# Performance work log

Hardware: AMD Instinct MI355X
Metric: run time of the kernel (lower is better)

## Reference

```python
import jax, jax.numpy as jnp
import numpy as np

B, S, D = 4, 2048, 1024
H = 16
HD = D // H  # 64


def setup_inputs() -> dict:
    key = jax.random.key(0)
    ks = jax.random.split(key, 6)
    scale = 1.0 / np.sqrt(D)
    return {
        "x": jax.random.normal(ks[0], (B, S, D), dtype=jnp.float32),
        "W_q": jax.random.normal(ks[1], (D, D), dtype=jnp.float32) * scale,
        "W_k": jax.random.normal(ks[2], (D, D), dtype=jnp.float32) * scale,
        "W_v": jax.random.normal(ks[3], (D, D), dtype=jnp.float32) * scale,
        "W_o": jax.random.normal(ks[4], (D, D), dtype=jnp.float32) * scale,
        "b_o": jax.random.normal(ks[5], (D,), dtype=jnp.float32) * 0.01,
    }


def reference(x, W_q, W_k, W_v, W_o, b_o):
    b, n, _ = x.shape
    # projections (Linear stores weight as [out,in]; here W_* are [in,out])
    q = (x @ W_q).reshape(b, n, H, HD).transpose(0, 2, 1, 3)  # [b,h,n,hd]
    k = (x @ W_k).reshape(b, n, H, HD).transpose(0, 2, 1, 3)
    v = (x @ W_v).reshape(b, n, H, HD).transpose(0, 2, 1, 3)
    scores = jnp.einsum("bhqd,bhkd->bhqk", q, k) / np.sqrt(HD).astype(np.float32)
    causal = jnp.tril(jnp.ones((n, n), dtype=bool))  # True = keep
    scores = jnp.where(causal, scores, -jnp.inf)
    weights = jax.nn.softmax(scores, axis=-1)
    ctx = jnp.einsum("bhqk,bhkd->bhqd", weights, v)
    ctx = ctx.transpose(0, 2, 1, 3).reshape(b, n, D)
    return ctx @ W_o + b_o
```

## Files before the change

### kernel.cpp

```cpp
#include <hip/hip_runtime.h>
#include <cstdint>

#define S_LEN 2048
#define D_MODEL 1024
#define NH 16
#define HDIM 64
#define BATCH 4

typedef __attribute__((ext_vector_type(8))) __bf16 bfrag;
typedef __attribute__((ext_vector_type(4))) float ffrag;

__device__ __forceinline__ unsigned short f2bf(float f) {
    union { float f; uint32_t u; } v; v.f = f;
    uint32_t u = v.u;
    u += 0x7fff + ((u >> 16) & 1);
    return (unsigned short)(u >> 16);
}

__device__ __forceinline__ bfrag ld_frag(const unsigned short* p) {
    union { uint4 u; bfrag b; } x;
    x.u = *(const uint4*)p;
    return x.b;
}

__device__ __forceinline__ float fast_exp2(float x) {
#if __has_builtin(__builtin_amdgcn_exp2f)
    return __builtin_amdgcn_exp2f(x);
#else
    return __expf(x * 0.6931471805599453f);
#endif
}

__device__ __forceinline__ uint32_t pack_bf16(float a, float b) {
    union { float f; uint32_t u; } x, y; x.f = a; y.f = b;
    return __builtin_amdgcn_perm(y.u + 0x8000u, x.u + 0x8000u, 0x07060302u);
}

__device__ __forceinline__ void g2l16(const unsigned short* g, unsigned short* l) {
    __builtin_amdgcn_global_load_lds(
        (const __attribute__((address_space(1))) void*)g,
        (__attribute__((address_space(3))) void*)l, 16, 0, 0);
}

__global__ __launch_bounds__(256) void prep_kernel(const float* __restrict__ x,
                                                   const float* __restrict__ w0,
                                                   const float* __restrict__ w1,
                                                   const float* __restrict__ w2,
                                                   const float* __restrict__ w3,
                                                   unsigned short* __restrict__ xb,
                                                   unsigned short* __restrict__ wt) {
    __shared__ float tile[32][33];
    int bid = blockIdx.x;
    int t = threadIdx.x;
    if (bid < 4096) {
        int i = bid * 256 + t;
        const float4* p = (const float4*)x + (size_t)i * 2;
        float4 a = p[0], b = p[1];
        union { unsigned short u[8]; uint4 v; } o;
        o.u[0]=f2bf(a.x); o.u[1]=f2bf(a.y); o.u[2]=f2bf(a.z); o.u[3]=f2bf(a.w);
        o.u[4]=f2bf(b.x); o.u[5]=f2bf(b.y); o.u[6]=f2bf(b.z); o.u[7]=f2bf(b.w);
        ((uint4*)xb)[i] = o.v;
    } else {
        int r = bid - 4096;
        int mat = r >> 10;
        int rem = r & 1023;
        const float* w = (mat == 0) ? w0 : (mat == 1) ? w1 : (mat == 2) ? w2 : w3;
        int n0 = (rem & 31) * 32, k0 = (rem >> 5) * 32;
        int tx = t & 31, ty = t >> 5;
        for (int i = 0; i < 32; i += 8)
            tile[ty + i][tx] = w[(size_t)(k0 + ty + i) * D_MODEL + n0 + tx];
        __syncthreads();
        unsigned short* o = wt + (size_t)mat * D_MODEL * D_MODEL;
        for (int i = 0; i < 32; i += 8)
            o[(size_t)(n0 + ty + i) * D_MODEL + (k0 + tx)] = f2bf(tile[tx][ty + i]);
    }
}

#define MFMA_BF16 __builtin_amdgcn_mfma_f32_16x16x32_bf16

__device__ __forceinline__ int vb_idx(int row, int col) {
    return row * 64 + (col & 7) +
           ((((col >> 3) ^ ((row >> 2) & 3) ^ ((row >> 4) & 3)) & 7) << 3);
}

#define AS_SLOT 8192
#define NKT  (D_MODEL / 32)

template<int NF, int MODE>
__global__ __launch_bounds__(512, 4) void gemm_kernel(
    const unsigned short* __restrict__ A,
    const unsigned short* __restrict__ Bt,
    unsigned short* __restrict__ Qb,
    unsigned short* __restrict__ Kb,
    unsigned short* __restrict__ Vtb,
    float* __restrict__ Out,
    const float* __restrict__ bias) {
    constexpr int BN = NF * 32;
    constexpr int BS_SLOT = BN * 32;
    constexpr int NBCH = BN * 4;
    constexpr int NWB = NBCH / 64;
    __shared__ unsigned short Smem[3 * AS_SLOT + 3 * BS_SLOT];
    unsigned short* As = Smem;
    unsigned short* Bs = Smem + 3 * AS_SLOT;
    int t = threadIdx.x;

    int gx   = (int)gridDim.x;
    int nwg  = gx * (int)gridDim.y;
    int flat = (int)(blockIdx.y * gridDim.x + blockIdx.x);
    int cpx  = nwg >> 3;
    int wid  = (flat & 7) * cpx + (flat >> 3);
    int m0 = (wid / gx) * 256;
    int n0 = (wid % gx) * BN;

    int wave = t >> 6, lane = t & 63;
    int quad = lane >> 4, lrow = lane & 15;
    int wr = (wave & 3) * 64;
    int wc = (wave >> 2) * (NF * 16);

    ffrag acc[4][NF];
    const ffrag fz = {0.f, 0.f, 0.f, 0.f};
#pragma unroll
    for (int i = 0; i < 4; i++)
#pragma unroll
        for (int j = 0; j < NF; j++) acc[i][j] = fz;

    int r0 = t >> 2,        g0 = (t & 3) ^ ((r0 >> 1) & 3);
    int c1 = 512 + t;
    int r1 = c1 >> 2,       g1 = (c1 & 3) ^ ((r1 >> 1) & 3);
    int cbi = t & (NBCH - 1);
    int rB = cbi >> 2,      gB = (cbi & 3) ^ ((rB >> 1) & 3);
    const unsigned short* pA0 = A  + (size_t)(m0 + r0) * D_MODEL + g0 * 8;
    const unsigned short* pA1 = A  + (size_t)(m0 + r1) * D_MODEL + g1 * 8;
    const unsigned short* pB0 = Bt + (size_t)(n0 + rB) * D_MODEL + gB * 8;
    unsigned short* lA0 = &As[(wave * 64) * 8];
    unsigned short* lA1 = &As[(512 + wave * 64) * 8];
    unsigned short* lB0 = &Bs[((wave & (NWB - 1)) * 64) * 8];

    g2l16(pA0, lA0);
    g2l16(pA1, lA1);
    g2l16(pB0, lB0);
    g2l16(pA0 + 32, lA0 + AS_SLOT);
    g2l16(pA1 + 32, lA1 + AS_SLOT);
    g2l16(pB0 + 32, lB0 + BS_SLOT);

    int aCur = 0, aNxt = AS_SLOT, aSpr = 2 * AS_SLOT;
    int bCur = 0, bNxt = BS_SLOT, bSpr = 2 * BS_SLOT;

    for (int kt = 0; kt < NKT - 1; ++kt) {
        asm volatile("s_waitcnt vmcnt(3)\n\ts_barrier" ::: "memory");
        __builtin_amdgcn_sched_barrier(0);
        if (kt + 2 < NKT) {
            int ko = (kt + 2) * 32;
            g2l16(pA0 + ko, lA0 + aSpr);
            g2l16(pA1 + ko, lA1 + aSpr);
            g2l16(pB0 + ko, lB0 + bSpr);
        }
        bfrag af[4], bf[NF];
#pragma unroll
        for (int ni = 0; ni < NF; ni++) {
            int row = wc + ni * 16 + lrow;
            bf[ni] = ld_frag(&Bs[bCur + row * 32 + ((quad ^ ((row >> 1) & 3)) * 8)]);
        }
#pragma unroll
        for (int mi = 0; mi < 4; mi++) {
            int row = wr + mi * 16 + lrow;
            af[mi] = ld_frag(&As[aCur + row * 32 + ((quad ^ ((row >> 1) & 3)) * 8)]);
        }
        __builtin_amdgcn_s_setprio(1);
#pragma unroll
        for (int mi = 0; mi < 4; mi++)
#pragma unroll
            for (int ni = 0; ni < NF; ni++)
                acc[mi][ni] = MFMA_BF16(af[mi], bf[ni], acc[mi][ni], 0, 0, 0);
        __builtin_amdgcn_s_setprio(0);
        int ta = aCur; aCur = aNxt; aNxt = aSpr; aSpr = ta;
        int tb = bCur; bCur = bNxt; bNxt = bSpr; bSpr = tb;
    }
    asm volatile("s_waitcnt vmcnt(0)\n\ts_barrier" ::: "memory");
    __builtin_amdgcn_sched_barrier(0);
    {
        bfrag af[4], bf[NF];
#pragma unroll
        for (int ni = 0; ni < NF; ni++) {
            int row = wc + ni * 16 + lrow;
            bf[ni] = ld_frag(&Bs[bCur + row * 32 + ((quad ^ ((row >> 1) & 3)) * 8)]);
        }
#pragma unroll
        for (int mi = 0; mi < 4; mi++) {
            int row = wr + mi * 16 + lrow;
            af[mi] = ld_frag(&As[aCur + row * 32 + ((quad ^ ((row >> 1) & 3)) * 8)]);
        }
#pragma unroll
        for (int mi = 0; mi < 4; mi++)
#pragma unroll
            for (int ni = 0; ni < NF; ni++)
                acc[mi][ni] = MFMA_BF16(af[mi], bf[ni], acc[mi][ni], 0, 0, 0);
    }

    if constexpr (MODE == 0) {
        int matid = n0 >> 10;
        if (matid == 2) {
            __syncthreads();
            unsigned short* Lw = &Smem[wave * (64 * 64)];
#pragma unroll
            for (int mi = 0; mi < 4; mi++)
#pragma unroll
                for (int ni = 0; ni < NF; ni++)
#pragma unroll
                    for (int r = 0; r < 4; r++)
                        Lw[vb_idx(mi * 16 + quad * 4 + r, ni * 16 + lrow)] =
                            f2bf(acc[mi][ni][r]);
            int h0 = ((n0 + wc) & 1023) >> 6;
            int bb = m0 >> 11;
            size_t bh = (size_t)bb * NH + h0;
            int sbase = (m0 + wr) & 2047;
            unsigned short* Vt = Vtb + bh * (size_t)HDIM * S_LEN;
#pragma unroll
            for (int p = 0; p < 4; p++) {
                int d  = (lane >> 2) + p * 16;
                int sc = (lane & 3) * 16;
                union { unsigned short u[16]; uint4 v[2]; } o;
#pragma unroll
                for (int i = 0; i < 16; i++) o.u[i] = Lw[vb_idx(sc + i, d)];
                unsigned short* dst = Vt + (size_t)d * S_LEN + sbase + sc;
                *(uint4*)(dst)     = o.v[0];
                *(uint4*)(dst + 8) = o.v[1];
            }
        } else {
#pragma unroll
            for (int mi = 0; mi < 4; mi++) {
                int row = m0 + wr + mi * 16 + quad * 4;
#pragma unroll
                for (int ni = 0; ni < NF; ni++) {
                    int col = n0 + wc + ni * 16 + lrow;
#pragma unroll
                    for (int r = 0; r < 4; r++) {
                        float v = acc[mi][ni][r];
                        int m = row + r;
                        int nn = col & 1023;
                        int h = nn >> 6, d = nn & 63;
                        int b = m >> 11, s = m & 2047;
                        size_t bh = (size_t)(b * NH + h);
                        if (matid == 0) Qb[(bh * S_LEN + s) * HDIM + d] = f2bf(v);
                        else            Kb[(bh * S_LEN + s) * HDIM + d] = f2bf(v);
                    }
                }
            }
        }
    } else {
#pragma unroll
        for (int mi = 0; mi < 4; mi++) {
            int row = m0 + wr + mi * 16 + quad * 4;
#pragma unroll
            for (int ni = 0; ni < NF; ni++) {
                int col = n0 + wc + ni * 16 + lrow;
#pragma unroll
                for (int r = 0; r < 4; r++) {
                    int m = row + r;
                    Out[(size_t)m * D_MODEL + col] = acc[mi][ni][r] + bias[col];
                }
            }
        }
    }
}

#define SCALE2 0.18033688f
#define CSHIFT 4.0f
#define KVBUF 4096

__global__ __launch_bounds__(256, 4) void attn_kernel(
    const unsigned short* __restrict__ Qb,
    const unsigned short* __restrict__ Kb,
    const unsigned short* __restrict__ Vtb,
    unsigned short* __restrict__ ctxb) {
    __shared__ unsigned short Ks[2 * KVBUF];
    __shared__ unsigned short Vs[2 * KVBUF];
    __shared__ unsigned short Ps[4 * 16 * 64];
    int flat = (int)(blockIdx.y * gridDim.x + blockIdx.x);
    int wid  = (flat & 7) * 128 + (flat >> 3);
    int bx = wid & 15;
    int bh = wid >> 4;
    int t = threadIdx.x;
    int wave = t >> 6, lane = t & 63;
    int quad = lane >> 4, lrow = lane & 15;
    int swz = lrow & 7;
    int ca = (quad ^ swz) * 8;
    int cb = ca ^ 32;

    union { uint4 u; bfrag b; } one_u;
    one_u.u.x = 0x3F803F80u; one_u.u.y = 0x3F803F80u;
    one_u.u.z = 0x3F803F80u; one_u.u.w = 0x3F803F80u;
    bfrag onef = one_u.b;

    const unsigned short* Qg = Qb + (size_t)bh * S_LEN * HDIM;
    const unsigned short* Kg = Kb + (size_t)bh * S_LEN * HDIM;
    const unsigned short* Vg = Vtb + (size_t)bh * HDIM * S_LEN;
    int b = bh >> 4, h = bh & 15;

    int c0 = t, c1 = 256 + t;
    int kr0 = c0 >> 3, kp0 = (c0 & 7) ^ (kr0 & 7);
    int kr1 = c1 >> 3, kp1 = (c1 & 7) ^ (kr1 & 7);
    const unsigned short* pK0 = Kg + (size_t)kr0 * HDIM + kp0 * 8;
    const unsigned short* pK1 = Kg + (size_t)kr1 * HDIM + kp1 * 8;
    const unsigned short* pV0 = Vg + (size_t)kr0 * S_LEN + kp0 * 8;
    const unsigned short* pV1 = Vg + (size_t)kr1 * S_LEN + kp1 * 8;
    unsigned short* lK0 = &Ks[(wave * 64) * 8];
    unsigned short* lK1 = &Ks[(256 + wave * 64) * 8];
    unsigned short* lV0 = &Vs[(wave * 64) * 8];
    unsigned short* lV1 = &Vs[(256 + wave * 64) * 8];
    unsigned short* Pw = &Ps[wave * 16 * 64];

    int x8 = (((lrow >> 1) & 3) << 1) | (((lrow >> 3) & 1) << 3);
    int ql = lane >> 3, cc = lane & 7;

    for (int ph = 0; ph < 2; ph++) {
        int qc = ph == 0 ? (31 - bx) : bx;
        int qw = qc * 64 + wave * 16;
        int nk = qc + 1;

        bfrag qf[2];
#pragma unroll
        for (int c = 0; c < 2; c++)
            qf[c] = ld_frag(Qg + (size_t)(qw + lrow) * HDIM + c * 32 + quad * 8);

        ffrag acc[4];
        ffrag acc_l;
        const ffrag fz = {0.f, 0.f, 0.f, 0.f};
#pragma unroll
        for (int d = 0; d < 4; d++) acc[d] = fz;
        acc_l = fz;

        __syncthreads();
        g2l16(pK0, lK0);
        g2l16(pK1, lK1);
        g2l16(pV0, lV0);
        g2l16(pV1, lV1);

        for (int kt = 0; kt < nk; kt++) {
            int kbase = kt * 64;
            int buf = (kt & 1) * KVBUF;
            __syncthreads();
            if (kt + 1 < nk) {
                int nb = ((kt + 1) & 1) * KVBUF;
                size_t krow_off = (size_t)(kbase + 64) * HDIM;
                g2l16(pK0 + krow_off, lK0 + nb);
                g2l16(pK1 + krow_off, lK1 + nb);
                g2l16(pV0 + kbase + 64, lV0 + nb);
                g2l16(pV1 + kbase + 64, lV1 + nb);
            }

            ffrag sf[4];
            __builtin_amdgcn_s_setprio(1);
#pragma unroll
            for (int ki = 0; ki < 4; ki++) {
                int krow = buf + (ki * 16 + lrow) * 64;
                bfrag ka = ld_frag(&Ks[krow + ca]);
                bfrag kb = ld_frag(&Ks[krow + cb]);
                ffrag s = fz;
                s = __builtin_amdgcn_mfma_f32_16x16x32_bf16(ka, qf[0], s, 0, 0, 0);
                s = __builtin_amdgcn_mfma_f32_16x16x32_bf16(kb, qf[1], s, 0, 0, 0);
                sf[ki] = s;
            }
            __builtin_amdgcn_s_setprio(0);

            int qg = qw + lrow;
            bool need_mask = (kt == nk - 1);
            float sv[16];
#pragma unroll
            for (int ki = 0; ki < 4; ki++)
#pragma unroll
                for (int r = 0; r < 4; r++) {
                    float v = sf[ki][r];
                    if (need_mask) {
                        int key = kbase + ki * 16 + quad * 4 + r;
                        v = (key <= qg) ? v : -3.0e38f;
                    }
                    sv[ki * 4 + r] = fast_exp2(__builtin_fmaf(v, SCALE2, -CSHIFT));
                }
            int prow = lrow * 64;
#pragma unroll
            for (int ki = 0; ki < 4; ki++) {
                uint2 w2;
                w2.x = pack_bf16(sv[ki * 4 + 0], sv[ki * 4 + 1]);
                w2.y = pack_bf16(sv[ki * 4 + 2], sv[ki * 4 + 3]);
                int pc = ((ki * 2 + (quad >> 1)) ^ swz) * 8 + (quad & 1) * 4;
                *(uint2*)&Pw[prow + pc] = w2;
            }

            bfrag pf0 = ld_frag(&Pw[prow + ca]);
            bfrag pf1 = ld_frag(&Pw[prow + cb]);
            acc_l = __builtin_amdgcn_mfma_f32_16x16x32_bf16(onef, pf0, acc_l, 0, 0, 0);
            acc_l = __builtin_amdgcn_mfma_f32_16x16x32_bf16(onef, pf1, acc_l, 0, 0, 0);
            __builtin_amdgcn_s_setprio(1);
#pragma unroll
            for (int di = 0; di < 4; di++) {
                int vrow = buf + (di * 16 + lrow) * 64;
                bfrag va = ld_frag(&Vs[vrow + ca]);
                bfrag vb = ld_frag(&Vs[vrow + cb]);
                acc[di] = __builtin_amdgcn_mfma_f32_16x16x32_bf16(va, pf0, acc[di], 0, 0, 0);
                acc[di] = __builtin_amdgcn_mfma_f32_16x16x32_bf16(vb, pf1, acc[di], 0, 0, 0);
            }
            __builtin_amdgcn_s_setprio(0);
        }

        float rl = __builtin_amdgcn_rcpf(acc_l[0]);
#pragma unroll
        for (int di = 0; di < 4; di++) {
            uint2 w2;
            w2.x = pack_bf16(acc[di][0] * rl, acc[di][1] * rl);
            w2.y = pack_bf16(acc[di][2] * rl, acc[di][3] * rl);
            int slot = (4 * di + quad) ^ x8;
            *(uint2*)&Pw[lrow * 64 + slot * 4] = w2;
        }
#pragma unroll
        for (int p = 0; p < 2; p++) {
            int r = p * 8 + ql;
            int rx = ((r >> 1) & 3) | ((r & 8) >> 1);
            uint4 vv = *(uint4*)&Pw[r * 64 + (cc ^ rx) * 8];
            int q = qw + p * 8 + ql;
            *(uint4*)(ctxb + ((size_t)b * S_LEN + q) * D_MODEL + h * HDIM + cc * 8) = vv;
        }
    }
}

extern "C" void kernel_launch(void* const* d_in, const int* in_sizes, int n_in,
                              void* d_out, int out_size, void* d_ws, size_t ws_size,
                              hipStream_t stream) {
    const float* x   = (const float*)d_in[0];
    const float* W_q = (const float*)d_in[1];
    const float* W_k = (const float*)d_in[2];
    const float* W_v = (const float*)d_in[3];
    const float* W_o = (const float*)d_in[4];
    const float* b_o = (const float*)d_in[5];
    float* out = (float*)d_out;

    unsigned short* xb   = (unsigned short*)d_ws;
    unsigned short* Wt   = xb + (size_t)8192 * 1024;
    unsigned short* Qb   = Wt + (size_t)4 * 1024 * 1024;
    unsigned short* Kb   = Qb + (size_t)64 * 2048 * 64;
    unsigned short* Vtb  = Kb + (size_t)64 * 2048 * 64;
    unsigned short* ctxb = Vtb + (size_t)64 * 2048 * 64;
    unsigned short* Wto  = Wt + (size_t)3 * 1024 * 1024;

    prep_kernel<<<8192, 256, 0, stream>>>(x, W_q, W_k, W_v, W_o, xb, Wt);
    gemm_kernel<4, 0><<<dim3(24, 32), 512, 0, stream>>>(xb, Wt, Qb, Kb, Vtb, nullptr, nullptr);
    attn_kernel<<<dim3(16, 64), 256, 0, stream>>>(Qb, Kb, Vtb, ctxb);
    gemm_kernel<2, 1><<<dim3(16, 32), 512, 0, stream>>>(ctxb, Wto, nullptr, nullptr, nullptr, out, b_o);
}
```

Baseline: 246.5 us.

## Switch GEMM to double-buffered LDS and raise occupancy target

The GEMM kernel's LDS staging drops from a three-slot ring to a two-slot double buffer, so each iteration now waits for all outstanding loads (vmcnt(0)) before computing. The V-transpose epilogue is split into two passes over half the LDS to fit the smaller allocation. Launch bounds rise from 4 to 6 blocks per CU, trading prefetch depth for more resident workgroups. This risks more exposed global-load latency and tighter register limits, and it adds extra barriers in the epilogue.

```diff
diff --git a/kernel.cpp b/kernel.cpp
--- a/kernel.cpp
+++ b/kernel.cpp
@@ -87,7 +87,7 @@
 #define NKT  (D_MODEL / 32)
 
 template<int NF, int MODE>
-__global__ __launch_bounds__(512, 4) void gemm_kernel(
+__global__ __launch_bounds__(512, 6) void gemm_kernel(
     const unsigned short* __restrict__ A,
     const unsigned short* __restrict__ Bt,
     unsigned short* __restrict__ Qb,
@@ -99,9 +99,9 @@
     constexpr int BS_SLOT = BN * 32;
     constexpr int NBCH = BN * 4;
     constexpr int NWB = NBCH / 64;
-    __shared__ unsigned short Smem[3 * AS_SLOT + 3 * BS_SLOT];
+    __shared__ unsigned short Smem[2 * AS_SLOT + 2 * BS_SLOT];
     unsigned short* As = Smem;
-    unsigned short* Bs = Smem + 3 * AS_SLOT;
+    unsigned short* Bs = Smem + 2 * AS_SLOT;
     int t = threadIdx.x;
 
     int gx   = (int)gridDim.x;
@@ -139,22 +139,19 @@
     g2l16(pA0, lA0);
     g2l16(pA1, lA1);
     g2l16(pB0, lB0);
-    g2l16(pA0 + 32, lA0 + AS_SLOT);
-    g2l16(pA1 + 32, lA1 + AS_SLOT);
-    g2l16(pB0 + 32, lB0 + BS_SLOT);
-
-    int aCur = 0, aNxt = AS_SLOT, aSpr = 2 * AS_SLOT;
-    int bCur = 0, bNxt = BS_SLOT, bSpr = 2 * BS_SLOT;
-
-    for (int kt = 0; kt < NKT - 1; ++kt) {
-        asm volatile("s_waitcnt vmcnt(3)\n\ts_barrier" ::: "memory");
+
+    for (int kt = 0; kt < NKT; ++kt) {
+        asm volatile("s_waitcnt vmcnt(0)\n\ts_barrier" ::: "memory");
         __builtin_amdgcn_sched_barrier(0);
-        if (kt + 2 < NKT) {
-            int ko = (kt + 2) * 32;
-            g2l16(pA0 + ko, lA0 + aSpr);
-            g2l16(pA1 + ko, lA1 + aSpr);
-            g2l16(pB0 + ko, lB0 + bSpr);
-        }
+        if (kt + 1 < NKT) {
+            int ko = (kt + 1) * 32;
+            int ns = (kt + 1) & 1;
+            g2l16(pA0 + ko, lA0 + ns * AS_SLOT);
+            g2l16(pA1 + ko, lA1 + ns * AS_SLOT);
+            g2l16(pB0 + ko, lB0 + ns * BS_SLOT);
+        }
+        int aCur = (kt & 1) * AS_SLOT;
+        int bCur = (kt & 1) * BS_SLOT;
         bfrag af[4], bf[NF];
 #pragma unroll
         for (int ni = 0; ni < NF; ni++) {
@@ -173,58 +170,42 @@
             for (int ni = 0; ni < NF; ni++)
                 acc[mi][ni] = MFMA_BF16(af[mi], bf[ni], acc[mi][ni], 0, 0, 0);
         __builtin_amdgcn_s_setprio(0);
-        int ta = aCur; aCur = aNxt; aNxt = aSpr; aSpr = ta;
-        int tb = bCur; bCur = bNxt; bNxt = bSpr; bSpr = tb;
-    }
-    asm volatile("s_waitcnt vmcnt(0)\n\ts_barrier" ::: "memory");
-    __builtin_amdgcn_sched_barrier(0);
-    {
-        bfrag af[4], bf[NF];
-#pragma unroll
-        for (int ni = 0; ni < NF; ni++) {
-            int row = wc + ni * 16 + lrow;
-            bf[ni] = ld_frag(&Bs[bCur + row * 32 + ((quad ^ ((row >> 1) & 3)) * 8)]);
-        }
-#pragma unroll
-        for (int mi = 0; mi < 4; mi++) {
-            int row = wr + mi * 16 + lrow;
-            af[mi] = ld_frag(&As[aCur + row * 32 + ((quad ^ ((row >> 1) & 3)) * 8)]);
-        }
-#pragma unroll
-        for (int mi = 0; mi < 4; mi++)
-#pragma unroll
-            for (int ni = 0; ni < NF; ni++)
-                acc[mi][ni] = MFMA_BF16(af[mi], bf[ni], acc[mi][ni], 0, 0, 0);
     }
 
     if constexpr (MODE == 0) {
         int matid = n0 >> 10;
         if (matid == 2) {
             __syncthreads();
-            unsigned short* Lw = &Smem[wave * (64 * 64)];
-#pragma unroll
-            for (int mi = 0; mi < 4; mi++)
-#pragma unroll
-                for (int ni = 0; ni < NF; ni++)
-#pragma unroll
-                    for (int r = 0; r < 4; r++)
-                        Lw[vb_idx(mi * 16 + quad * 4 + r, ni * 16 + lrow)] =
-                            f2bf(acc[mi][ni][r]);
+            unsigned short* Lw = &Smem[(wave & 3) * (64 * 64)];
             int h0 = ((n0 + wc) & 1023) >> 6;
             int bb = m0 >> 11;
             size_t bh = (size_t)bb * NH + h0;
             int sbase = (m0 + wr) & 2047;
             unsigned short* Vt = Vtb + bh * (size_t)HDIM * S_LEN;
 #pragma unroll
-            for (int p = 0; p < 4; p++) {
-                int d  = (lane >> 2) + p * 16;
-                int sc = (lane & 3) * 16;
-                union { unsigned short u[16]; uint4 v[2]; } o;
-#pragma unroll
-                for (int i = 0; i < 16; i++) o.u[i] = Lw[vb_idx(sc + i, d)];
-                unsigned short* dst = Vt + (size_t)d * S_LEN + sbase + sc;
-                *(uint4*)(dst)     = o.v[0];
-                *(uint4*)(dst + 8) = o.v[1];
+            for (int pass = 0; pass < 2; pass++) {
+                if ((wave >> 2) == pass) {
+#pragma unroll
+                    for (int mi = 0; mi < 4; mi++)
+#pragma unroll
+                        for (int ni = 0; ni < NF; ni++)
+#pragma unroll
+                            for (int r = 0; r < 4; r++)
+                                Lw[vb_idx(mi * 16 + quad * 4 + r, ni * 16 + lrow)] =
+                                    f2bf(acc[mi][ni][r]);
+#pragma unroll
+                    for (int p = 0; p < 4; p++) {
+                        int d  = (lane >> 2) + p * 16;
+                        int sc = (lane & 3) * 16;
+                        union { unsigned short u[16]; uint4 v[2]; } o;
+#pragma unroll
+                        for (int i = 0; i < 16; i++) o.u[i] = Lw[vb_idx(sc + i, d)];
+                        unsigned short* dst = Vt + (size_t)d * S_LEN + sbase + sc;
+                        *(uint4*)(dst)     = o.v[0];
+                        *(uint4*)(dst + 8) = o.v[1];
+                    }
+                }
+                __syncthreads();
             }
         } else {
 #pragma unroll
```

Result: slower. 560.9 us (+127.6%).
